# Performance work log

Measured on AMD Instinct MI355X. Metric: run time of the kernel, lower is better.

Reference implementation:

```python
import jax, jax.numpy as jnp
import numpy as np
from jax import lax

B_COEF = 0.25  # commitment loss weight
NUM_EMB = 1024
EMB_DIM = 64


def setup_inputs() -> dict:
    key = jax.random.key(0)
    k1, k2 = jax.random.split(key)
    z_e = jax.random.normal(k1, (32, EMB_DIM, 64, 64), dtype=jnp.float32)
    # codebook init: uniform(-1/num_emb, 1/num_emb) as in torch module
    emb = jax.random.uniform(k2, (NUM_EMB, EMB_DIM), dtype=jnp.float32,
                             minval=-1.0 / NUM_EMB, maxval=1.0 / NUM_EMB)
    return {"z_e": z_e, "emb": emb}


def reference(z_e, emb):
    b, c, h, w = z_e.shape  # c == emb_dim
    # (b,c,h,w) -> (b*h*w, c)
    z_flat = jnp.transpose(z_e, (0, 2, 3, 1)).reshape(b * h * w, c)
    # squared euclidean distance: ||z||^2 + ||e||^2 - 2 z.e^T
    dist = (jnp.sum(z_flat ** 2, axis=-1, keepdims=True)
            + jnp.sum(emb ** 2, axis=-1)[None, :]
            - 2.0 * jnp.matmul(z_flat, emb.T))
    enc_idx = jnp.argmin(dist, axis=-1)  # [b*h*w]
    z_q = emb[enc_idx].reshape(b, h, w, c)  # gather
    z_q = jnp.transpose(z_q, (0, 3, 1, 2))  # (b,c,h,w)
    reconstruction_loss = jnp.mean((z_q - lax.stop_gradient(z_e)) ** 2)
    commitment_loss = B_COEF * jnp.mean((lax.stop_gradient(z_q) - z_e) ** 2)
    loss = reconstruction_loss + commitment_loss
    # straight-through estimator
    z_q_st = z_e + lax.stop_gradient(z_q - z_e)
    return z_q_st, loss, enc_idx
```

## Files before the change

kernel.cpp:

```cpp
#include <hip/hip_runtime.h>
#include <hip/hip_bf16.h>

#define NUM_EMB 1024
#define EMB_DIM 64
#define NPIX    131072
#define ZQ_ELEMS 8388608
#define KDEPTH  16
#define ZSTRIDE 65
#define NACC    64
#define BIAS    0.25f


typedef __attribute__((ext_vector_type(8))) short short8_t;
typedef __attribute__((ext_vector_type(4))) float f32x4;

__device__ __forceinline__ unsigned umin32(unsigned a, unsigned b) { return a < b ? a : b; }
__device__ __forceinline__ unsigned umax32(unsigned a, unsigned b) { return a > b ? a : b; }

__global__ void vq_zero_ws(float* __restrict__ loss_out, float* __restrict__ wsAcc) {
    if (threadIdx.x == 0) loss_out[0] = 0.f;
    wsAcc[threadIdx.x] = 0.f;
}

__device__ __forceinline__ float np_sumsq64(const float* __restrict__ x) {
    float q[EMB_DIM];
    #pragma unroll
    for (int c = 0; c < EMB_DIM; ++c) q[c] = x[c] * x[c];
    float r0 = q[0], r1 = q[1], r2 = q[2], r3 = q[3];
    float r4 = q[4], r5 = q[5], r6 = q[6], r7 = q[7];
    #pragma unroll
    for (int g = 1; g < 8; ++g) {
        r0 += q[8 * g + 0]; r1 += q[8 * g + 1];
        r2 += q[8 * g + 2]; r3 += q[8 * g + 3];
        r4 += q[8 * g + 4]; r5 += q[8 * g + 5];
        r6 += q[8 * g + 6]; r7 += q[8 * g + 7];
    }
    return ((r0 + r1) + (r2 + r3)) + ((r4 + r5) + (r6 + r7));
}

__device__ __forceinline__ unsigned long long packvk(float v, int k) {
    unsigned u = __float_as_uint(v);
    u = (u & 0x80000000u) ? ~u : (u | 0x80000000u);
    return ((unsigned long long)u << 32) | (unsigned)k;
}

__global__ __launch_bounds__(256) void vq_prep(const float* __restrict__ emb,
                                               short* __restrict__ wsE,
                                               float* __restrict__ wsE2) {
    #pragma clang fp contract(off)
    int t    = blockIdx.x * 256 + threadIdx.x;
    int l    = t & 63;
    int ch   = (t >> 6) & 15;
    int q    = t >> 10;
    int code = q * 256 + ch * 16 + (l & 15);
    const float* ek = emb + code * EMB_DIM;
    #pragma unroll
    for (int h = 0; h < 2; ++h) {
        short8_t pk;
        #pragma unroll
        for (int j = 0; j < 8; ++j) {
            int chan = 32 * h + 8 * (l >> 4) + j;
            __hip_bfloat16 bv = __float2bfloat16(-2.0f * ek[chan]);
            unsigned short u; __builtin_memcpy(&u, &bv, 2);
            pk[j] = (short)u;
        }
        *(short8_t*)(wsE + t * 16 + h * 8) = pk;
    }
    if (t < NUM_EMB) wsE2[t] = np_sumsq64(emb + t * EMB_DIM);
}

__global__ __launch_bounds__(256, 4) void vq_mfma(const float* __restrict__ z_e,
                                                  const float* __restrict__ emb,
                                                  const short* __restrict__ wsE,
                                                  const float* __restrict__ wsE2,
                                                  float* __restrict__ zq_out,
                                                  float* __restrict__ enc_out,
                                                  float* __restrict__ wsAcc) {
    #pragma clang fp contract(off)
    __shared__ float sZf[64 * ZSTRIDE];
    __shared__ float sE2[NUM_EMB];
    __shared__ float sE2b[NUM_EMB];
    __shared__ unsigned sMinP[4][64];
    __shared__ float sBand[64];
    __shared__ float sThrF[64];
    __shared__ unsigned sThrP[64];
    __shared__ float sZZ[64];
    __shared__ unsigned long long sBestPack[64];
    __shared__ unsigned short sKbuf[64][KDEPTH];
    __shared__ int   sKcnt[64];
    __shared__ int   sPxFlag[64];
    __shared__ int   sFlagAny;

    const int tid  = threadIdx.x;
    const int w    = tid >> 6;
    const int lane = tid & 63;
    const int p0   = blockIdx.x * 64;
    const int b    = p0 >> 12;
    const int hw0  = p0 & 4095;
    const float* base = z_e + (size_t)b * (EMB_DIM * 4096) + hw0;

    {
        f32x4 e2x = *(const f32x4*)&wsE2[tid * 4];
        *(f32x4*)&sE2[tid * 4] = e2x;
        f32x4 eb;
        eb[0] = e2x[0] + BIAS; eb[1] = e2x[1] + BIAS;
        eb[2] = e2x[2] + BIAS; eb[3] = e2x[3] + BIAS;
        *(f32x4*)&sE2b[tid * 4] = eb;
    }
    if (tid < 64) { sKcnt[tid] = 0; sBestPack[tid] = ~0ULL; sPxFlag[tid] = 0; }
    if (tid == 0) sFlagAny = 0;

    {
        const float* zp = base + lane;
        float v[16];
        #pragma unroll
        for (int j = 0; j < 16; ++j) v[j] = zp[(size_t)(16 * w + j) * 4096];
        #pragma unroll
        for (int j = 0; j < 16; ++j) sZf[lane * ZSTRIDE + 16 * w + j] = v[j];
    }
    __syncthreads();

    if (w == 0) {
        const float* zl = &sZf[lane * ZSTRIDE];
        float rr[8] = {0,0,0,0,0,0,0,0};
        float sab = 0.f;
        #pragma unroll
        for (int g = 0; g < 8; ++g)
            #pragma unroll
            for (int j = 0; j < 8; ++j) {
                float zc = zl[8 * g + j];
                float qq = zc * zc;
                rr[j] += qq;
                sab += fabsf(zc);
            }
        sZZ[lane]   = ((rr[0] + rr[1]) + (rr[2] + rr[3])) + ((rr[4] + rr[5]) + (rr[6] + rr[7]));
        sBand[lane] = 2.0f * (9e-6f * sab + 2e-5f) + 1e-4f;
    }

    short8_t bfrag[4][2];
    #pragma unroll
    for (int pg = 0; pg < 4; ++pg)
        #pragma unroll
        for (int h = 0; h < 2; ++h) {
            int bpr = pg * 16 + (lane & 15);
            int c0  = 32 * h + 8 * (lane >> 4);
            short8_t pk;
            #pragma unroll
            for (int j = 0; j < 8; ++j) {
                __hip_bfloat16 bv = __float2bfloat16(sZf[bpr * ZSTRIDE + c0 + j]);
                unsigned short u; __builtin_memcpy(&u, &bv, 2);
                pk[j] = (short)u;
            }
            asm volatile("" : "+v"(pk));
            bfrag[pg][h] = pk;
        }

    const short8_t* ef = (const short8_t*)wsE + (size_t)w * 2048;

    unsigned p1[4] = {~0u, ~0u, ~0u, ~0u};
    unsigned p2[4] = {~0u, ~0u, ~0u, ~0u};
    unsigned p3[4] = {~0u, ~0u, ~0u, ~0u};
    {
        short8_t A0 = ef[lane * 2 + 0];
        short8_t A1 = ef[lane * 2 + 1];
        #pragma unroll 1
        for (int ch = 0; ch < 16; ++ch) {
            int chn = ch < 15 ? ch + 1 : 15;
            short8_t N0 = ef[(chn * 64 + lane) * 2 + 0];
            short8_t N1 = ef[(chn * 64 + lane) * 2 + 1];
            int kbase = w * 256 + ch * 16 + 4 * (lane >> 4);
            f32x4 e2bv = *(const f32x4*)(&sE2b[kbase]);
            unsigned kb[4] = {(unsigned)kbase, (unsigned)kbase + 1u,
                              (unsigned)kbase + 2u, (unsigned)kbase + 3u};
            #pragma unroll
            for (int pg = 0; pg < 4; ++pg) {
                f32x4 acc = __builtin_amdgcn_mfma_f32_16x16x32_bf16(A0, bfrag[pg][0], e2bv, 0, 0, 0);
                acc = __builtin_amdgcn_mfma_f32_16x16x32_bf16(A1, bfrag[pg][1], acc, 0, 0, 0);
                #pragma unroll
                for (int j = 0; j < 4; ++j) {
                    unsigned t  = (__float_as_uint(acc[j]) & 0xFFFFFC00u) | kb[j];
                    unsigned n1 = umin32(p1[pg], t);
                    unsigned x1 = umax32(p1[pg], t);
                    unsigned n2 = umin32(p2[pg], x1);
                    unsigned x2 = umax32(p2[pg], x1);
                    unsigned n3 = umin32(p3[pg], x2);
                    p1[pg] = n1; p2[pg] = n2; p3[pg] = n3;
                }
            }
            A0 = N0; A1 = N1;
        }
    }

    #pragma unroll
    for (int pg = 0; pg < 4; ++pg) {
        unsigned g = p1[pg];
        g = umin32(g, (unsigned)__shfl_xor((int)g, 16, 64));
        g = umin32(g, (unsigned)__shfl_xor((int)g, 32, 64));
        if (lane < 16) sMinP[w][pg * 16 + lane] = g;
    }
    __syncthreads();
    if (tid < 64) {
        unsigned gp = umin32(umin32(sMinP[0][tid], sMinP[1][tid]),
                             umin32(sMinP[2][tid], sMinP[3][tid]));
        float m    = __uint_as_float(gp & 0xFFFFFC00u);
        float thrF = m + sBand[tid];
        sThrF[tid] = thrF;
        sThrP[tid] = (__float_as_uint(thrF) & 0xFFFFFC00u) | 1023u;
    }
    __syncthreads();

    #pragma unroll
    for (int pg = 0; pg < 4; ++pg) {
        int px = pg * 16 + (lane & 15);
        unsigned thrp = sThrP[px];
        if (p1[pg] <= thrp) {
            int slot = atomicAdd(&sKcnt[px], 1);
            if (slot < KDEPTH) sKbuf[px][slot] = (unsigned short)(p1[pg] & 1023u);
        }
        if (p2[pg] <= thrp) {
            int slot = atomicAdd(&sKcnt[px], 1);
            if (slot < KDEPTH) sKbuf[px][slot] = (unsigned short)(p2[pg] & 1023u);
        }
        if (p3[pg] <= thrp) {
            int slot = atomicAdd(&sKcnt[px], 1);
            if (slot < KDEPTH) sKbuf[px][slot] = (unsigned short)(p3[pg] & 1023u);
            sPxFlag[px] = 1; sFlagAny = 1;
        }
    }
    __syncthreads();

    if (sFlagAny) {
        if (tid < 64 && sPxFlag[tid]) sKcnt[tid] = 0;
        __syncthreads();
        float thrB[4];
        #pragma unroll
        for (int pg = 0; pg < 4; ++pg) {
            int px = pg * 16 + (lane & 15);
            thrB[pg] = sPxFlag[px] ? sThrF[px] : -1e30f;
        }
        short8_t A0 = ef[lane * 2 + 0];
        short8_t A1 = ef[lane * 2 + 1];
        #pragma unroll 1
        for (int ch = 0; ch < 16; ++ch) {
            int chn = ch < 15 ? ch + 1 : 15;
            short8_t N0 = ef[(chn * 64 + lane) * 2 + 0];
            short8_t N1 = ef[(chn * 64 + lane) * 2 + 1];
            int kbase = w * 256 + ch * 16 + 4 * (lane >> 4);
            f32x4 e2bv = *(const f32x4*)(&sE2b[kbase]);
            #pragma unroll
            for (int pg = 0; pg < 4; ++pg) {
                f32x4 acc = __builtin_amdgcn_mfma_f32_16x16x32_bf16(A0, bfrag[pg][0], e2bv, 0, 0, 0);
                acc = __builtin_amdgcn_mfma_f32_16x16x32_bf16(A1, bfrag[pg][1], acc, 0, 0, 0);
                #pragma unroll
                for (int j = 0; j < 4; ++j) {
                    if (acc[j] <= thrB[pg]) {
                        int pix  = pg * 16 + (lane & 15);
                        int slot = atomicAdd(&sKcnt[pix], 1);
                        if (slot < KDEPTH) sKbuf[pix][slot] = (unsigned short)(kbase + j);
                    }
                }
            }
            A0 = N0; A1 = N1;
        }
        __syncthreads();
    }

    {
        const int px = lane;
        const float* zl = &sZf[px * ZSTRIDE];
        float zzv = sZZ[px];
        int rawcnt = sKcnt[px];
        if (rawcnt == 1) {
            if (w == 0) sBestPack[px] = packvk(-1e30f, (int)sKbuf[px][0]);
        } else if (rawcnt <= KDEPTH) {
            for (int s = w; s < rawcnt; s += 4) {
                int k = (int)sKbuf[px][s];
                const float* ek = emb + k * EMB_DIM;
                float acc = 0.f;
                #pragma unroll 8
                for (int c = 0; c < EMB_DIM; ++c)
                    acc = fmaf(ek[c], zl[c], acc);
                float v = (zzv + sE2[k]) - 2.0f * acc;
                atomicMin(&sBestPack[px], packvk(v, k));
            }
        } else {
            for (int k = w; k < NUM_EMB; k += 4) {
                const float* ek = emb + k * EMB_DIM;
                float acc = 0.f;
                #pragma unroll 8
                for (int c = 0; c < EMB_DIM; ++c)
                    acc = fmaf(ek[c], zl[c], acc);
                float v = (zzv + sE2[k]) - 2.0f * acc;
                atomicMin(&sBestPack[px], packvk(v, k));
            }
        }
    }
    __syncthreads();

    if (tid < 64)
        enc_out[p0 + tid] = (float)(unsigned)(sBestPack[tid] & 0xFFFFFFFFull);
    {
        const int px = lane;
        int bestk = (int)(sBestPack[px] & 0xFFFFFFFFull);
        const float* eq = emb + bestk * EMB_DIM;
        const float* zl = &sZf[px * ZSTRIDE];
        float* op = zq_out + (size_t)b * (EMB_DIM * 4096) + hw0 + px;
        float ls = 0.f;
        #pragma unroll
        for (int j = 0; j < 16; ++j) {
            int c = 16 * w + j;
            float qv = eq[c];
            float d = qv - zl[c];
            ls = fmaf(d, d, ls);
            op[(size_t)c * 4096] = qv;
        }
        #pragma unroll
        for (int off = 32; off > 0; off >>= 1) ls += __shfl_down(ls, off, 64);
        if (lane == 0) atomicAdd(&wsAcc[blockIdx.x & (NACC - 1)], ls);
    }
}

__global__ void vq_final_ws(const float* __restrict__ wsAcc,
                            float* __restrict__ loss_out) {
    int lane = threadIdx.x;
    float v = wsAcc[lane];
    #pragma unroll
    for (int off = 32; off > 0; off >>= 1) v += __shfl_down(v, off, 64);
    if (lane == 0) loss_out[0] = v * (1.25f / (float)ZQ_ELEMS);
}

__global__ void vq_final_direct(float* __restrict__ loss_out) {
    loss_out[0] = loss_out[0] * (1.25f / (float)ZQ_ELEMS);
}

__global__ __launch_bounds__(256) void vq_nn_fb(const float* __restrict__ z_e,
                                                const float* __restrict__ emb,
                                                float* __restrict__ zq_out,
                                                float* __restrict__ enc_out,
                                                float* __restrict__ loss_acc) {
    #pragma clang fp contract(off)
    __shared__ float s_e2[NUM_EMB];
    int tid = threadIdx.x;
    for (int k = tid; k < NUM_EMB; k += 256) s_e2[k] = np_sumsq64(emb + k * EMB_DIM);
    __syncthreads();
    int p = blockIdx.x * 256 + tid;
    int b = p >> 12, hw = p & 4095;
    const float* zp = z_e + (size_t)b * (EMB_DIM * 4096) + hw;
    float z[EMB_DIM];
    #pragma unroll
    for (int c = 0; c < EMB_DIM; ++c) z[c] = zp[(size_t)c * 4096];
    float zz = np_sumsq64(z);
    float b1 = 3.4e38f; int i1 = 0;
    #pragma unroll 2
    for (int k = 0; k < NUM_EMB; ++k) {
        const float* ek = emb + k * EMB_DIM;
        float acc = 0.f;
        #pragma unroll
        for (int c = 0; c < EMB_DIM; ++c) acc = fmaf(ek[c], z[c], acc);
        float sc = (zz + s_e2[k]) - 2.0f * acc;
        bool lt = sc < b1; b1 = lt ? sc : b1; i1 = lt ? k : i1;
    }
    const float* eq = emb + i1 * EMB_DIM;
    float* op = zq_out + (size_t)b * (EMB_DIM * 4096) + hw;
    float ls = 0.f;
    #pragma unroll
    for (int c = 0; c < EMB_DIM; ++c) {
        float q = eq[c]; float d = q - z[c];
        ls = fmaf(d, d, ls);
        op[(size_t)c * 4096] = q;
    }
    enc_out[p] = (float)i1;
    #pragma unroll
    for (int off = 32; off > 0; off >>= 1) ls += __shfl_down(ls, off, 64);
    if ((tid & 63) == 0) atomicAdd(loss_acc, ls);
}

extern "C" void kernel_launch(void* const* d_in, const int* in_sizes, int n_in,
                              void* d_out, int out_size, void* d_ws, size_t ws_size,
                              hipStream_t stream) {
    const float* z_e = (const float*)d_in[0];
    const float* emb = (const float*)d_in[1];
    float* out = (float*)d_out;
    float* loss_out = out + ZQ_ELEMS;
    float* enc_out  = out + ZQ_ELEMS + 1;

    if (ws_size >= 140 * 1024) {
        short* wsE   = (short*)d_ws;
        float* wsE2  = (float*)((char*)d_ws + 131072);
        float* wsAcc = (float*)((char*)d_ws + 135168);
        vq_zero_ws<<<1, NACC, 0, stream>>>(loss_out, wsAcc);
        vq_prep<<<16, 256, 0, stream>>>(emb, wsE, wsE2);
        vq_mfma<<<NPIX / 64, 256, 0, stream>>>(z_e, emb, wsE, wsE2, out, enc_out, wsAcc);
        vq_final_ws<<<1, 64, 0, stream>>>(wsAcc, loss_out);
    } else {
        hipMemsetAsync(loss_out, 0, 4, stream);
        vq_nn_fb<<<NPIX / 256, 256, 0, stream>>>(z_e, emb, out, enc_out, loss_out);
        vq_final_direct<<<1, 1, 0, stream>>>(loss_out);
    }
}
```

Before: 92.45 us.

## Fold zeroing and final loss reduction into neighbouring kernels, raise occupancy

Removes the separate zero-init kernel by clearing the accumulators in vq_prep, and replaces the final reduction kernel with a last-block-done pattern using a global atomic counter inside vq_mfma. It also drops the biased e2 shared array, adding the bias in registers to cut LDS use, and raises the launch-bounds occupancy hint from 4 to 6. This is meant to cut two kernel launches and allow more resident blocks, at the cost of extra threadfences and a global atomic per block, plus possible register pressure or spills.

```diff
diff --git a/kernel.cpp b/kernel.cpp
--- a/kernel.cpp
+++ b/kernel.cpp
@@ -9,6 +9,7 @@
 #define ZSTRIDE 65
 #define NACC    64
 #define BIAS    0.25f
+#define NBLK    (NPIX / 64)
 
 
 typedef __attribute__((ext_vector_type(8))) short short8_t;
@@ -16,11 +17,6 @@
 
 __device__ __forceinline__ unsigned umin32(unsigned a, unsigned b) { return a < b ? a : b; }
 __device__ __forceinline__ unsigned umax32(unsigned a, unsigned b) { return a > b ? a : b; }
-
-__global__ void vq_zero_ws(float* __restrict__ loss_out, float* __restrict__ wsAcc) {
-    if (threadIdx.x == 0) loss_out[0] = 0.f;
-    wsAcc[threadIdx.x] = 0.f;
-}
 
 __device__ __forceinline__ float np_sumsq64(const float* __restrict__ x) {
     float q[EMB_DIM];
@@ -46,9 +42,15 @@
 
 __global__ __launch_bounds__(256) void vq_prep(const float* __restrict__ emb,
                                                short* __restrict__ wsE,
-                                               float* __restrict__ wsE2) {
+                                               float* __restrict__ wsE2,
+                                               float* __restrict__ wsAcc,
+                                               int* __restrict__ wsDone) {
     #pragma clang fp contract(off)
     int t    = blockIdx.x * 256 + threadIdx.x;
+    if (blockIdx.x == 0) {
+        if (threadIdx.x < NACC) wsAcc[threadIdx.x] = 0.f;
+        if (threadIdx.x == 0) wsDone[0] = 0;
+    }
     int l    = t & 63;
     int ch   = (t >> 6) & 15;
     int q    = t >> 10;
@@ -69,17 +71,18 @@
     if (t < NUM_EMB) wsE2[t] = np_sumsq64(emb + t * EMB_DIM);
 }
 
-__global__ __launch_bounds__(256, 4) void vq_mfma(const float* __restrict__ z_e,
+__global__ __launch_bounds__(256, 6) void vq_mfma(const float* __restrict__ z_e,
                                                   const float* __restrict__ emb,
                                                   const short* __restrict__ wsE,
                                                   const float* __restrict__ wsE2,
                                                   float* __restrict__ zq_out,
                                                   float* __restrict__ enc_out,
-                                                  float* __restrict__ wsAcc) {
+                                                  float* __restrict__ wsAcc,
+                                                  int* __restrict__ wsDone,
+                                                  float* __restrict__ loss_out) {
     #pragma clang fp contract(off)
     __shared__ float sZf[64 * ZSTRIDE];
     __shared__ float sE2[NUM_EMB];
-    __shared__ float sE2b[NUM_EMB];
     __shared__ unsigned sMinP[4][64];
     __shared__ float sBand[64];
     __shared__ float sThrF[64];
@@ -90,6 +93,7 @@
     __shared__ int   sKcnt[64];
     __shared__ int   sPxFlag[64];
     __shared__ int   sFlagAny;
+    __shared__ int   sIsLast;
 
     const int tid  = threadIdx.x;
     const int w    = tid >> 6;
@@ -99,14 +103,7 @@
     const int hw0  = p0 & 4095;
     const float* base = z_e + (size_t)b * (EMB_DIM * 4096) + hw0;
 
-    {
-        f32x4 e2x = *(const f32x4*)&wsE2[tid * 4];
-        *(f32x4*)&sE2[tid * 4] = e2x;
-        f32x4 eb;
-        eb[0] = e2x[0] + BIAS; eb[1] = e2x[1] + BIAS;
-        eb[2] = e2x[2] + BIAS; eb[3] = e2x[3] + BIAS;
-        *(f32x4*)&sE2b[tid * 4] = eb;
-    }
+    *(f32x4*)&sE2[tid * 4] = *(const f32x4*)&wsE2[tid * 4];
     if (tid < 64) { sKcnt[tid] = 0; sBestPack[tid] = ~0ULL; sPxFlag[tid] = 0; }
     if (tid == 0) sFlagAny = 0;
 
@@ -169,7 +166,10 @@
             short8_t N0 = ef[(chn * 64 + lane) * 2 + 0];
             short8_t N1 = ef[(chn * 64 + lane) * 2 + 1];
             int kbase = w * 256 + ch * 16 + 4 * (lane >> 4);
-            f32x4 e2bv = *(const f32x4*)(&sE2b[kbase]);
+            f32x4 e2v = *(const f32x4*)(&sE2[kbase]);
+            f32x4 e2bv;
+            e2bv[0] = e2v[0] + BIAS; e2bv[1] = e2v[1] + BIAS;
+            e2bv[2] = e2v[2] + BIAS; e2bv[3] = e2v[3] + BIAS;
             unsigned kb[4] = {(unsigned)kbase, (unsigned)kbase + 1u,
                               (unsigned)kbase + 2u, (unsigned)kbase + 3u};
             #pragma unroll
@@ -246,7 +246,10 @@
             short8_t N0 = ef[(chn * 64 + lane) * 2 + 0];
             short8_t N1 = ef[(chn * 64 + lane) * 2 + 1];
             int kbase = w * 256 + ch * 16 + 4 * (lane >> 4);
-            f32x4 e2bv = *(const f32x4*)(&sE2b[kbase]);
+            f32x4 e2v = *(const f32x4*)(&sE2[kbase]);
+            f32x4 e2bv;
+            e2bv[0] = e2v[0] + BIAS; e2bv[1] = e2v[1] + BIAS;
+            e2bv[2] = e2v[2] + BIAS; e2bv[3] = e2v[3] + BIAS;
             #pragma unroll
             for (int pg = 0; pg < 4; ++pg) {
                 f32x4 acc = __builtin_amdgcn_mfma_f32_16x16x32_bf16(A0, bfrag[pg][0], e2bv, 0, 0, 0);
@@ -318,15 +321,17 @@
         for (int off = 32; off > 0; off >>= 1) ls += __shfl_down(ls, off, 64);
         if (lane == 0) atomicAdd(&wsAcc[blockIdx.x & (NACC - 1)], ls);
     }
-}
-
-__global__ void vq_final_ws(const float* __restrict__ wsAcc,
-                            float* __restrict__ loss_out) {
-    int lane = threadIdx.x;
-    float v = wsAcc[lane];
-    #pragma unroll
-    for (int off = 32; off > 0; off >>= 1) v += __shfl_down(v, off, 64);
-    if (lane == 0) loss_out[0] = v * (1.25f / (float)ZQ_ELEMS);
+
+    __threadfence();
+    if (tid == 0) sIsLast = (atomicAdd(wsDone, 1) == NBLK - 1);
+    __syncthreads();
+    if (sIsLast && w == 0) {
+        __threadfence();
+        float v = wsAcc[lane];
+        #pragma unroll
+        for (int off = 32; off > 0; off >>= 1) v += __shfl_down(v, off, 64);
+        if (lane == 0) loss_out[0] = v * (1.25f / (float)ZQ_ELEMS);
+    }
 }
 
 __global__ void vq_final_direct(float* __restrict__ loss_out) {
@@ -388,10 +393,10 @@
         short* wsE   = (short*)d_ws;
         float* wsE2  = (float*)((char*)d_ws + 131072);
         float* wsAcc = (float*)((char*)d_ws + 135168);
-        vq_zero_ws<<<1, NACC, 0, stream>>>(loss_out, wsAcc);
-        vq_prep<<<16, 256, 0, stream>>>(emb, wsE, wsE2);
-        vq_mfma<<<NPIX / 64, 256, 0, stream>>>(z_e, emb, wsE, wsE2, out, enc_out, wsAcc);
-        vq_final_ws<<<1, 64, 0, stream>>>(wsAcc, loss_out);
+        int*   wsDone= (int*)  ((char*)d_ws + 135424);
+        vq_prep<<<16, 256, 0, stream>>>(emb, wsE, wsE2, wsAcc, wsDone);
+        vq_mfma<<<NBLK, 256, 0, stream>>>(z_e, emb, wsE, wsE2, out, enc_out,
+                                          wsAcc, wsDone, loss_out);
     } else {
         hipMemsetAsync(loss_out, 0, 4, stream);
         vq_nn_fb<<<NPIX / 256, 256, 0, stream>>>(z_e, emb, out, enc_out, loss_out);
```

New measurement: 267.1 us. 189% more time.
